# Optimization experiments

Measured on AMD Instinct MI355X. Metric: run time of the kernel, lower is better.

Reference implementation:

```python
import jax, jax.numpy as jnp
import numpy as np

N, K, D = 262144, 1024, 64

def setup_inputs() -> dict:
    key = jax.random.key(0)
    k1, k2 = jax.random.split(key)
    previous_residual = jax.random.normal(k1, (N, D), dtype=jnp.float32)
    # GlorotUniform over (K, D): limit = sqrt(6/(K+D))
    limit = np.sqrt(6.0 / (K + D)).astype(np.float32)
    codebook_embeddings = jax.random.uniform(k2, (K, D), dtype=jnp.float32, minval=-limit, maxval=limit)
    return {"previous_residual": previous_residual, "codebook_embeddings": codebook_embeddings}

def reference(previous_residual, codebook_embeddings):
    x_sq = jnp.sum(previous_residual * previous_residual, axis=-1, keepdims=True)  # [N,1]
    c_sq = jnp.sum(codebook_embeddings * codebook_embeddings, axis=-1)             # [K]
    xc = jnp.einsum('nd,kd->nk', previous_residual, codebook_embeddings)           # [N,K]
    distances = x_sq - 2.0 * xc + c_sq[None, :]
    closest_codebook_index = jnp.argmin(distances, axis=1)                          # [N] int
    codebook_embedding = codebook_embeddings[closest_codebook_index]                # [N,D]
    next_residual = previous_residual - codebook_embedding
    return (closest_codebook_index, next_residual, codebook_embedding)
```

## Files before the change

kernel.cpp:

```cpp
#include <hip/hip_runtime.h>
#include <math.h>

#define N_ROWS 262144
#define K_CODES 1024
#define D_DIM 64
#define WL_CAP 262144

typedef __attribute__((ext_vector_type(8))) short short8;
typedef __attribute__((ext_vector_type(4))) float f32x4;
typedef unsigned short ushortT;
typedef unsigned int uintT;

__device__ inline uintT bf16_rne_bits(float v) {
    uintT u = __float_as_uint(v);
    return (u + 0x7FFFu + ((u >> 16) & 1u)) >> 16;
}

__global__ __launch_bounds__(64) void prep_kernel(const float* __restrict__ cb,
                                                  ushortT* __restrict__ cbh,
                                                  ushortT* __restrict__ cbl,
                                                  float* __restrict__ c_sq,
                                                  int* __restrict__ cnt) {
    if (blockIdx.x == 0 && threadIdx.x == 0) *cnt = 0;
    int k = blockIdx.x * 64 + threadIdx.x;
    if (k >= K_CODES) return;
    const float4* row = (const float4*)(cb + (size_t)k * D_DIM);
    float s = 0.0f;
#pragma unroll
    for (int j = 0; j < D_DIM / 4; ++j) {
        float4 v = row[j];
        s = fmaf(v.x, v.x, s);
        s = fmaf(v.y, v.y, s);
        s = fmaf(v.z, v.z, s);
        s = fmaf(v.w, v.w, s);
        float e[4] = {v.x, v.y, v.z, v.w};
#pragma unroll
        for (int q = 0; q < 4; ++q) {
            int d = 4 * j + q;
            uintT hb = bf16_rne_bits(e[q]);
            float hif = __uint_as_float(hb << 16);
            uintT lb = bf16_rne_bits(e[q] - hif);
            cbh[(size_t)k * D_DIM + d] = (ushortT)hb;
            cbl[(size_t)k * D_DIM + d] = (ushortT)lb;
        }
    }
    c_sq[k] = s;
}

__global__ __launch_bounds__(256, 4) void coarse_kernel(
        const float* __restrict__ x_all, const float* __restrict__ cb,
        const ushortT* __restrict__ cbh, const ushortT* __restrict__ cbl,
        const float* __restrict__ c_sq_g,
        float* __restrict__ out_idx, float* __restrict__ out_res,
        float* __restrict__ out_emb, int* __restrict__ cnt,
        int* __restrict__ wl) {
    __shared__ __align__(16) ushortT stage[8192];
    __shared__ float csq_s[K_CODES];
    __shared__ float xsq_s[128];
    __shared__ int   idx_s[128];

    const int t  = threadIdx.x;
    const int w  = t >> 6;
    const int L  = t & 63;
    const int q  = L >> 4;
    const int n  = L & 15;
    const int rowbase = blockIdx.x * 128 + w * 32;

    ((float4*)csq_s)[t] = ((const float4*)c_sq_g)[t];

    short8 ah[2][2], al[2][2];
#pragma unroll
    for (int s = 0; s < 2; ++s) {
        float part = 0.0f;
#pragma unroll
        for (int kt = 0; kt < 2; ++kt) {
            const float4* p = (const float4*)(x_all +
                (size_t)(rowbase + s * 16 + n) * D_DIM + kt * 32 + q * 8);
            float4 v0 = p[0], v1 = p[1];
            float e[8] = {v0.x, v0.y, v0.z, v0.w, v1.x, v1.y, v1.z, v1.w};
#pragma unroll
            for (int j = 0; j < 8; ++j) {
                part = fmaf(e[j], e[j], part);
                uintT hb = bf16_rne_bits(e[j]);
                float hif = __uint_as_float(hb << 16);
                uintT lb = bf16_rne_bits(e[j] - hif);
                ah[s][kt][j] = (short)hb;
                al[s][kt][j] = (short)lb;
            }
        }
        part += __shfl_xor(part, 16);
        part += __shfl_xor(part, 32);
        if (q == 0) xsq_s[w * 32 + s * 16 + n] = part;
    }

    uint4 pre[4];
#pragma unroll
    for (int i = 0; i < 4; ++i) {
        int c = i * 256 + t;
        int tile = c >> 8, inner = c & 255;
        int hilo = inner >> 7, cc = inner & 127;
        int kt = cc >> 6, LL = cc & 63;
        const ushortT* src = hilo ? cbl : cbh;
        size_t elem = (size_t)(tile * 16 + (LL & 15)) * D_DIM + kt * 32 + (LL >> 4) * 8;
        pre[i] = *(const uint4*)(src + elem);
    }

    int m1p[2][4], m2p[2][4];
#pragma unroll
    for (int s = 0; s < 2; ++s)
#pragma unroll
        for (int j = 0; j < 4; ++j) { m1p[s][j] = (int)0x80000000; m2p[s][j] = (int)0x80000000; }

    for (int r = 0; r < 16; ++r) {
        __syncthreads();
#pragma unroll
        for (int i = 0; i < 4; ++i)
            *(uint4*)(stage + (size_t)(i * 256 + t) * 8) = pre[i];
        __syncthreads();

        if (r < 15) {
            int rn = r + 1;
#pragma unroll
            for (int i = 0; i < 4; ++i) {
                int c = i * 256 + t;
                int tile = c >> 8, inner = c & 255;
                int hilo = inner >> 7, cc = inner & 127;
                int kt = cc >> 6, LL = cc & 63;
                const ushortT* src = hilo ? cbl : cbh;
                size_t elem = (size_t)(rn * 64 + tile * 16 + (LL & 15)) * D_DIM +
                              kt * 32 + (LL >> 4) * 8;
                pre[i] = *(const uint4*)(src + elem);
            }
        }

#pragma unroll
        for (int tl = 0; tl < 4; ++tl) {
            const int tb = tl * 2048;
            short8 bh0 = *(const short8*)(stage + tb +    0 + L * 8);
            short8 bh1 = *(const short8*)(stage + tb +  512 + L * 8);
            short8 bl0 = *(const short8*)(stage + tb + 1024 + L * 8);
            short8 bl1 = *(const short8*)(stage + tb + 1536 + L * 8);

            f32x4 p0 = {0.f,0.f,0.f,0.f}, q0 = {0.f,0.f,0.f,0.f};
            f32x4 p1 = {0.f,0.f,0.f,0.f}, q1 = {0.f,0.f,0.f,0.f};
            p0 = __builtin_amdgcn_mfma_f32_16x16x32_bf16(ah[0][0], bh0, p0, 0, 0, 0);
            p1 = __builtin_amdgcn_mfma_f32_16x16x32_bf16(ah[1][0], bh0, p1, 0, 0, 0);
            q0 = __builtin_amdgcn_mfma_f32_16x16x32_bf16(ah[0][1], bl1, q0, 0, 0, 0);
            q1 = __builtin_amdgcn_mfma_f32_16x16x32_bf16(ah[1][1], bl1, q1, 0, 0, 0);
            p0 = __builtin_amdgcn_mfma_f32_16x16x32_bf16(ah[0][1], bh1, p0, 0, 0, 0);
            p1 = __builtin_amdgcn_mfma_f32_16x16x32_bf16(ah[1][1], bh1, p1, 0, 0, 0);
            q0 = __builtin_amdgcn_mfma_f32_16x16x32_bf16(al[0][0], bh0, q0, 0, 0, 0);
            q1 = __builtin_amdgcn_mfma_f32_16x16x32_bf16(al[1][0], bh0, q1, 0, 0, 0);
            p0 = __builtin_amdgcn_mfma_f32_16x16x32_bf16(ah[0][0], bl0, p0, 0, 0, 0);
            p1 = __builtin_amdgcn_mfma_f32_16x16x32_bf16(ah[1][0], bl0, p1, 0, 0, 0);
            q0 = __builtin_amdgcn_mfma_f32_16x16x32_bf16(al[0][1], bh1, q0, 0, 0, 0);
            q1 = __builtin_amdgcn_mfma_f32_16x16x32_bf16(al[1][1], bh1, q1, 0, 0, 0);
            f32x4 s0 = p0 + q0;
            f32x4 s1 = p1 + q1;

            int tg = r * 4 + tl;
            float cv = csq_s[tg * 16 + n];
            uintT kcp = (uintT)(63 - tg);
#pragma unroll
            for (int j = 0; j < 4; ++j) {
                float v0 = fmaf(2.0f, s0[j], -cv);
                int u0 = (int)((__float_as_uint(v0) & 0xFFFFFFC0u) | kcp);
                m2p[0][j] = max(m2p[0][j], min(m1p[0][j], u0));
                m1p[0][j] = max(m1p[0][j], u0);
                float v1 = fmaf(2.0f, s1[j], -cv);
                int u1 = (int)((__float_as_uint(v1) & 0xFFFFFFC0u) | kcp);
                m2p[1][j] = max(m2p[1][j], min(m1p[1][j], u1));
                m1p[1][j] = max(m1p[1][j], u1);
            }
        }
    }

#pragma unroll
    for (int s = 0; s < 2; ++s)
#pragma unroll
        for (int j = 0; j < 4; ++j) {
            int p1i = m1p[s][j], p2i = m2p[s][j];
            float a1 = __uint_as_float((uintT)p1i & 0xFFFFFFC0u);
            float a2 = __uint_as_float((uintT)p2i & 0xFFFFFFC0u);
            int ai = ((63 - (p1i & 63)) << 4) | n;
#pragma unroll
            for (int msk = 1; msk < 16; msk <<= 1) {
                float o1 = __shfl_xor(a1, msk);
                float o2 = __shfl_xor(a2, msk);
                int oi = __shfl_xor(ai, msk);
                float nm2 = fmaxf(fminf(a1, o1), fmaxf(a2, o2));
                bool take = (o1 > a1) || (o1 == a1 && oi < ai);
                a1 = take ? o1 : a1;
                ai = take ? oi : ai;
                a2 = nm2;
            }
            if (n == 0) {
                int rl = w * 32 + s * 16 + q * 4 + j;
                float xsq = xsq_s[rl];
                float xn = sqrtf(xsq);
                float thr = fmaf(8.0e-5f, xn, 6.44140625e-4f);
                bool fb = ((a1 - a2) <= thr) || (a2 < 0.0f) || (xsq > 170.0f);
                idx_s[rl] = ai | (fb ? (1 << 30) : 0);
            }
        }
    __syncthreads();

    if (t < 128) {
        int e = idx_s[t];
        int row = blockIdx.x * 128 + t;
        out_idx[row] = (float)(e & 0x3FFFFFFF);
        if (e >> 30) {
            int pos = atomicAdd(cnt, 1);
            if (pos < WL_CAP) wl[pos] = row;
        }
    }
    {
        int lr = t >> 1;
        int row = blockIdx.x * 128 + lr;
        int seg = (t & 1) * 32;
        int id = idx_s[lr] & 0x3FFFFFFF;
        const float4* xs = (const float4*)(x_all + (size_t)row * D_DIM + seg);
        const float4* cs = (const float4*)(cb + (size_t)id * D_DIM + seg);
        float4* rs = (float4*)(out_res + (size_t)row * D_DIM + seg);
        float4* es = (float4*)(out_emb + (size_t)row * D_DIM + seg);
#pragma unroll
        for (int j = 0; j < 8; ++j) {
            float4 xv = xs[j], cv = cs[j];
            float4 rv;
            rv.x = xv.x - cv.x; rv.y = xv.y - cv.y;
            rv.z = xv.z - cv.z; rv.w = xv.w - cv.w;
            rs[j] = rv;
            es[j] = cv;
        }
    }
}

__global__ __launch_bounds__(256) void fallback_kernel(
        const float* __restrict__ x_all, const float* __restrict__ cb,
        const float* __restrict__ c_sq, const int* __restrict__ wl,
        const int* __restrict__ cnt,
        float* __restrict__ out_idx, float* __restrict__ out_res,
        float* __restrict__ out_emb) {
    int count = *cnt;
    if (count > WL_CAP) count = WL_CAP;
    const int L = threadIdx.x & 63;
    const int waveId = blockIdx.x * 4 + (threadIdx.x >> 6);
    const int nWaves = gridDim.x * 4;

    for (int i = waveId; i < count; i += nWaves) {
        int r = wl[i];

        float x[D_DIM];
        const float4* xr = (const float4*)(x_all + (size_t)r * D_DIM);
#pragma unroll
        for (int j = 0; j < D_DIM / 4; ++j) {
            float4 v = xr[j];
            x[4 * j + 0] = v.x; x[4 * j + 1] = v.y;
            x[4 * j + 2] = v.z; x[4 * j + 3] = v.w;
        }
        float x_sq = 0.0f;
#pragma unroll
        for (int d = 0; d < D_DIM; ++d) x_sq = fmaf(x[d], x[d], x_sq);

        float best = INFINITY;
        int bidx = 0x7FFFFFFF;
        for (int kk = 0; kk < 16; ++kk) {
            int k = kk * 64 + L;
            const float* c0 = cb + (size_t)k * D_DIM;
            float a00 = 0.f, a01 = 0.f, a02 = 0.f, a03 = 0.f;
#pragma unroll
            for (int j = 0; j < 4; ++j) {
                float4 v0 = *(const float4*)(c0 + 16 * j + 0);
                float4 v1 = *(const float4*)(c0 + 16 * j + 4);
                float4 v2 = *(const float4*)(c0 + 16 * j + 8);
                float4 v3 = *(const float4*)(c0 + 16 * j + 12);
                float* a = (j == 0) ? &a00 : (j == 1) ? &a01 : (j == 2) ? &a02 : &a03;
                float acc = *a;
                acc = fmaf(x[16 * j + 0],  v0.x, acc);
                acc = fmaf(x[16 * j + 1],  v0.y, acc);
                acc = fmaf(x[16 * j + 2],  v0.z, acc);
                acc = fmaf(x[16 * j + 3],  v0.w, acc);
                acc = fmaf(x[16 * j + 4],  v1.x, acc);
                acc = fmaf(x[16 * j + 5],  v1.y, acc);
                acc = fmaf(x[16 * j + 6],  v1.z, acc);
                acc = fmaf(x[16 * j + 7],  v1.w, acc);
                acc = fmaf(x[16 * j + 8],  v2.x, acc);
                acc = fmaf(x[16 * j + 9],  v2.y, acc);
                acc = fmaf(x[16 * j + 10], v2.z, acc);
                acc = fmaf(x[16 * j + 11], v2.w, acc);
                acc = fmaf(x[16 * j + 12], v3.x, acc);
                acc = fmaf(x[16 * j + 13], v3.y, acc);
                acc = fmaf(x[16 * j + 14], v3.z, acc);
                acc = fmaf(x[16 * j + 15], v3.w, acc);
                *a = acc;
            }
            float dot = (a00 + a01) + (a02 + a03);
            float d = (x_sq - 2.0f * dot) + c_sq[k];
            if (d < best) { best = d; bidx = k; }
        }

#pragma unroll
        for (int msk = 1; msk < 64; msk <<= 1) {
            float ob = __shfl_xor(best, msk);
            int oi = __shfl_xor(bidx, msk);
            bool take = (ob < best) || (ob == best && oi < bidx);
            best = take ? ob : best;
            bidx = take ? oi : bidx;
        }

        if (L < 16) {
            const float4* cbest = (const float4*)(cb + (size_t)bidx * D_DIM);
            float4 c = cbest[L];
            float4 v;
            v.x = x[4 * L + 0] - c.x; v.y = x[4 * L + 1] - c.y;
            v.z = x[4 * L + 2] - c.z; v.w = x[4 * L + 3] - c.w;
            ((float4*)(out_res + (size_t)r * D_DIM))[L] = v;
            ((float4*)(out_emb + (size_t)r * D_DIM))[L] = c;
            if (L == 0) out_idx[r] = (float)bidx;
        }
    }
}

extern "C" void kernel_launch(void* const* d_in, const int* in_sizes, int n_in,
                              void* d_out, int out_size, void* d_ws, size_t ws_size,
                              hipStream_t stream) {
    const float* x  = (const float*)d_in[0];
    const float* cb = (const float*)d_in[1];

    char* base = (char*)d_ws;
    ushortT* cbh = (ushortT*)base;
    ushortT* cbl = (ushortT*)(base + 131072);
    float*   csq = (float*)(base + 262144);
    int*     cnt = (int*)(base + 266240);
    int*     wl  = (int*)(base + 266256);

    float* out   = (float*)d_out;
    float* o_idx = out;
    float* o_res = out + (size_t)N_ROWS;
    float* o_emb = o_res + (size_t)N_ROWS * D_DIM;

    prep_kernel<<<16, 64, 0, stream>>>(cb, cbh, cbl, csq, cnt);
    coarse_kernel<<<N_ROWS / 128, 256, 0, stream>>>(x, cb, cbh, cbl, csq,
                                                    o_idx, o_res, o_emb, cnt, wl);
    fallback_kernel<<<1024, 256, 0, stream>>>(x, cb, csq, wl, cnt,
                                              o_idx, o_res, o_emb);
}
```

Before: 451.2 us.

## Double-buffer codebook staging and fuse ambiguous-row fallback into coarse kernel

```diff
diff --git a/kernel.cpp b/kernel.cpp
--- a/kernel.cpp
+++ b/kernel.cpp
@@ -4,7 +4,6 @@
 #define N_ROWS 262144
 #define K_CODES 1024
 #define D_DIM 64
-#define WL_CAP 262144
 
 typedef __attribute__((ext_vector_type(8))) short short8;
 typedef __attribute__((ext_vector_type(4))) float f32x4;
@@ -19,9 +18,7 @@
 __global__ __launch_bounds__(64) void prep_kernel(const float* __restrict__ cb,
                                                   ushortT* __restrict__ cbh,
                                                   ushortT* __restrict__ cbl,
-                                                  float* __restrict__ c_sq,
-                                                  int* __restrict__ cnt) {
-    if (blockIdx.x == 0 && threadIdx.x == 0) *cnt = 0;
+                                                  float* __restrict__ c_sq) {
     int k = blockIdx.x * 64 + threadIdx.x;
     if (k >= K_CODES) return;
     const float4* row = (const float4*)(cb + (size_t)k * D_DIM);
@@ -52,9 +49,8 @@
         const ushortT* __restrict__ cbh, const ushortT* __restrict__ cbl,
         const float* __restrict__ c_sq_g,
         float* __restrict__ out_idx, float* __restrict__ out_res,
-        float* __restrict__ out_emb, int* __restrict__ cnt,
-        int* __restrict__ wl) {
-    __shared__ __align__(16) ushortT stage[8192];
+        float* __restrict__ out_emb) {
+    __shared__ __align__(16) ushortT stage[2][8192];
     __shared__ float csq_s[K_CODES];
     __shared__ float xsq_s[128];
     __shared__ int   idx_s[128];
@@ -93,17 +89,29 @@
         if (q == 0) xsq_s[w * 32 + s * 16 + n] = part;
     }
 
+    auto fetch = [&](int rr, uint4* pre) {
+#pragma unroll
+        for (int i = 0; i < 4; ++i) {
+            int c = i * 256 + t;
+            int tile = c >> 8, inner = c & 255;
+            int hilo = inner >> 7, cc = inner & 127;
+            int kt = cc >> 6, LL = cc & 63;
+            const ushortT* src = hilo ? cbl : cbh;
+            size_t elem = (size_t)(rr * 64 + tile * 16 + (LL & 15)) * D_DIM +
+                          kt * 32 + (LL >> 4) * 8;
+            pre[i] = *(const uint4*)(src + elem);
+        }
+    };
+    auto store_stage = [&](int b, const uint4* pre) {
+#pragma unroll
+        for (int i = 0; i < 4; ++i)
+            *(uint4*)(&stage[b][(size_t)(i * 256 + t) * 8]) = pre[i];
+    };
+
     uint4 pre[4];
-#pragma unroll
-    for (int i = 0; i < 4; ++i) {
-        int c = i * 256 + t;
-        int tile = c >> 8, inner = c & 255;
-        int hilo = inner >> 7, cc = inner & 127;
-        int kt = cc >> 6, LL = cc & 63;
-        const ushortT* src = hilo ? cbl : cbh;
-        size_t elem = (size_t)(tile * 16 + (LL & 15)) * D_DIM + kt * 32 + (LL >> 4) * 8;
-        pre[i] = *(const uint4*)(src + elem);
-    }
+    fetch(0, pre);
+    store_stage(0, pre);
+    fetch(1, pre);
 
     int m1p[2][4], m2p[2][4];
 #pragma unroll
@@ -111,35 +119,17 @@
 #pragma unroll
         for (int j = 0; j < 4; ++j) { m1p[s][j] = (int)0x80000000; m2p[s][j] = (int)0x80000000; }
 
+    __syncthreads();
+
     for (int r = 0; r < 16; ++r) {
-        __syncthreads();
-#pragma unroll
-        for (int i = 0; i < 4; ++i)
-            *(uint4*)(stage + (size_t)(i * 256 + t) * 8) = pre[i];
-        __syncthreads();
-
-        if (r < 15) {
-            int rn = r + 1;
-#pragma unroll
-            for (int i = 0; i < 4; ++i) {
-                int c = i * 256 + t;
-                int tile = c >> 8, inner = c & 255;
-                int hilo = inner >> 7, cc = inner & 127;
-                int kt = cc >> 6, LL = cc & 63;
-                const ushortT* src = hilo ? cbl : cbh;
-                size_t elem = (size_t)(rn * 64 + tile * 16 + (LL & 15)) * D_DIM +
-                              kt * 32 + (LL >> 4) * 8;
-                pre[i] = *(const uint4*)(src + elem);
-            }
-        }
-
+        const ushortT* sb = stage[r & 1];
 #pragma unroll
         for (int tl = 0; tl < 4; ++tl) {
             const int tb = tl * 2048;
-            short8 bh0 = *(const short8*)(stage + tb +    0 + L * 8);
-            short8 bh1 = *(const short8*)(stage + tb +  512 + L * 8);
-            short8 bl0 = *(const short8*)(stage + tb + 1024 + L * 8);
-            short8 bl1 = *(const short8*)(stage + tb + 1536 + L * 8);
+            short8 bh0 = *(const short8*)(sb + tb +    0 + L * 8);
+            short8 bh1 = *(const short8*)(sb + tb +  512 + L * 8);
+            short8 bl0 = *(const short8*)(sb + tb + 1024 + L * 8);
+            short8 bl1 = *(const short8*)(sb + tb + 1536 + L * 8);
 
             f32x4 p0 = {0.f,0.f,0.f,0.f}, q0 = {0.f,0.f,0.f,0.f};
             f32x4 p1 = {0.f,0.f,0.f,0.f}, q1 = {0.f,0.f,0.f,0.f};
@@ -173,6 +163,11 @@
                 m1p[1][j] = max(m1p[1][j], u1);
             }
         }
+        if (r < 15) {
+            store_stage((r + 1) & 1, pre);
+            if (r < 14) fetch(r + 2, pre);
+        }
+        __syncthreads();
     }
 
 #pragma unroll
@@ -207,51 +202,34 @@
 
     if (t < 128) {
         int e = idx_s[t];
-        int row = blockIdx.x * 128 + t;
-        out_idx[row] = (float)(e & 0x3FFFFFFF);
-        if (e >> 30) {
-            int pos = atomicAdd(cnt, 1);
-            if (pos < WL_CAP) wl[pos] = row;
-        }
-    }
-    {
-        int lr = t >> 1;
-        int row = blockIdx.x * 128 + lr;
-        int seg = (t & 1) * 32;
-        int id = idx_s[lr] & 0x3FFFFFFF;
-        const float4* xs = (const float4*)(x_all + (size_t)row * D_DIM + seg);
-        const float4* cs = (const float4*)(cb + (size_t)id * D_DIM + seg);
-        float4* rs = (float4*)(out_res + (size_t)row * D_DIM + seg);
-        float4* es = (float4*)(out_emb + (size_t)row * D_DIM + seg);
-#pragma unroll
-        for (int j = 0; j < 8; ++j) {
-            float4 xv = xs[j], cv = cs[j];
-            float4 rv;
-            rv.x = xv.x - cv.x; rv.y = xv.y - cv.y;
-            rv.z = xv.z - cv.z; rv.w = xv.w - cv.w;
-            rs[j] = rv;
-            es[j] = cv;
-        }
-    }
-}
-
-__global__ __launch_bounds__(256) void fallback_kernel(
-        const float* __restrict__ x_all, const float* __restrict__ cb,
-        const float* __restrict__ c_sq, const int* __restrict__ wl,
-        const int* __restrict__ cnt,
-        float* __restrict__ out_idx, float* __restrict__ out_res,
-        float* __restrict__ out_emb) {
-    int count = *cnt;
-    if (count > WL_CAP) count = WL_CAP;
-    const int L = threadIdx.x & 63;
-    const int waveId = blockIdx.x * 4 + (threadIdx.x >> 6);
-    const int nWaves = gridDim.x * 4;
-
-    for (int i = waveId; i < count; i += nWaves) {
-        int r = wl[i];
+        if (!(e >> 30)) out_idx[blockIdx.x * 128 + t] = (float)(e & 0x3FFFFFFF);
+    }
+#pragma unroll
+    for (int c2 = 0; c2 < 8; ++c2) {
+        int f = c2 * 256 + t;
+        int lr = f >> 4;
+        int e = idx_s[lr];
+        if (e >> 30) continue;
+        int id = e & 0x3FFFFFFF;
+        size_t row = (size_t)blockIdx.x * 128 + lr;
+        int el = f & 15;
+        float4 xv = ((const float4*)(x_all + row * D_DIM))[el];
+        float4 cv = ((const float4*)(cb + (size_t)id * D_DIM))[el];
+        float4 rv;
+        rv.x = xv.x - cv.x; rv.y = xv.y - cv.y;
+        rv.z = xv.z - cv.z; rv.w = xv.w - cv.w;
+        ((float4*)(out_res + row * D_DIM))[el] = rv;
+        ((float4*)(out_emb + row * D_DIM))[el] = cv;
+    }
+
+    for (int rr = 0; rr < 32; ++rr) {
+        int lr = w * 32 + rr;
+        int e = idx_s[lr];
+        if (!(e >> 30)) continue;
+        size_t row = (size_t)blockIdx.x * 128 + lr;
 
         float x[D_DIM];
-        const float4* xr = (const float4*)(x_all + (size_t)r * D_DIM);
+        const float4* xr = (const float4*)(x_all + row * D_DIM);
 #pragma unroll
         for (int j = 0; j < D_DIM / 4; ++j) {
             float4 v = xr[j];
@@ -295,7 +273,7 @@
                 *a = acc;
             }
             float dot = (a00 + a01) + (a02 + a03);
-            float d = (x_sq - 2.0f * dot) + c_sq[k];
+            float d = (x_sq - 2.0f * dot) + csq_s[k];
             if (d < best) { best = d; bidx = k; }
         }
 
@@ -314,9 +292,9 @@
             float4 v;
             v.x = x[4 * L + 0] - c.x; v.y = x[4 * L + 1] - c.y;
             v.z = x[4 * L + 2] - c.z; v.w = x[4 * L + 3] - c.w;
-            ((float4*)(out_res + (size_t)r * D_DIM))[L] = v;
-            ((float4*)(out_emb + (size_t)r * D_DIM))[L] = c;
-            if (L == 0) out_idx[r] = (float)bidx;
+            ((float4*)(out_res + row * D_DIM))[L] = v;
+            ((float4*)(out_emb + row * D_DIM))[L] = c;
+            if (L == 0) out_idx[row] = (float)bidx;
         }
     }
 }
@@ -331,17 +309,13 @@
     ushortT* cbh = (ushortT*)base;
     ushortT* cbl = (ushortT*)(base + 131072);
     float*   csq = (float*)(base + 262144);
-    int*     cnt = (int*)(base + 266240);
-    int*     wl  = (int*)(base + 266256);
 
     float* out   = (float*)d_out;
     float* o_idx = out;
     float* o_res = out + (size_t)N_ROWS;
     float* o_emb = o_res + (size_t)N_ROWS * D_DIM;
 
-    prep_kernel<<<16, 64, 0, stream>>>(cb, cbh, cbl, csq, cnt);
+    prep_kernel<<<16, 64, 0, stream>>>(cb, cbh, cbl, csq);
     coarse_kernel<<<N_ROWS / 128, 256, 0, stream>>>(x, cb, cbh, cbl, csq,
-                                                    o_idx, o_res, o_emb, cnt, wl);
-    fallback_kernel<<<1024, 256, 0, stream>>>(x, cb, csq, wl, cnt,
-                                              o_idx, o_res, o_emb);
+                                                    o_idx, o_res, o_emb);
 }
```

After: 515.6 us. 14.3% more time.
